# Kernel tuning notes

Hardware: AMD Instinct MI355X
Metric: run time of the kernel (lower is better)

The kernel has to match this reference:

```python
import jax, jax.numpy as jnp
import numpy as np

B = 131072      # number of graphs
P = 22          # num_players (pad/truncate target)
F = 14          # num_features
N = B * P       # total nodes
H1, H2 = 256, 128


def setup_inputs() -> dict:
    key = jax.random.key(0)
    ks = jax.random.split(key, 8)
    x = jax.random.normal(ks[0], (N, F), dtype=jnp.float32)
    batch = jnp.sort(jax.random.randint(ks[1], (N,), 0, B, dtype=jnp.int32))
    s1 = 1.0 / np.sqrt(P * F)
    s2 = 1.0 / np.sqrt(H1)
    s3 = 1.0 / np.sqrt(H2)
    W1 = jax.random.uniform(ks[2], (H1, P * F), jnp.float32, -s1, s1)
    b1 = jax.random.uniform(ks[3], (H1,), jnp.float32, -s1, s1)
    W2 = jax.random.uniform(ks[4], (H2, H1), jnp.float32, -s2, s2)
    b2 = jax.random.uniform(ks[5], (H2,), jnp.float32, -s2, s2)
    W3 = jax.random.uniform(ks[6], (P, H2), jnp.float32, -s3, s3)
    b3 = jax.random.uniform(ks[7], (P,), jnp.float32, -s3, s3)
    return {"x": x, "batch": batch, "W1": W1, "b1": b1, "W2": W2, "b2": b2, "W3": W3, "b3": b3}


def _flatten_batch(x, batch):
    # Vectorized equivalent of the per-graph mask/slice/pad loop.
    counts = jax.ops.segment_sum(jnp.ones((N,), jnp.int32), batch, num_segments=B)
    starts = jnp.concatenate([jnp.zeros((1,), jnp.int32), jnp.cumsum(counts)[:-1].astype(jnp.int32)])
    pos = jnp.arange(N, dtype=jnp.int32) - starts[batch]  # position within own graph
    # nodes beyond the first P per graph are truncated -> route to dump slot P
    slot = jnp.where(pos < P, pos, P)
    buf = jnp.zeros((B, P + 1, F), dtype=x.dtype)          # zero padding for short graphs
    buf = buf.at[batch, slot].set(x)
    return buf[:, :P, :].reshape(B, P * F)


def reference(x, batch, W1, b1, W2, b2, W3, b3):
    flat = _flatten_batch(x, batch)                        # [B, 308]
    h1 = jax.nn.relu(flat @ W1.T + b1)                     # dropout is eval-mode identity
    h2 = jax.nn.relu(h1 @ W2.T + b2)
    logits = h2 @ W3.T + b3                                # [B, 22]
    return logits
```

## Files before the change

kernel.cpp:

```cpp
#include <hip/hip_runtime.h>
#include <hip/hip_fp16.h>

typedef __attribute__((ext_vector_type(8))) _Float16 half8;
typedef __attribute__((ext_vector_type(4))) float f32x4;

namespace {
constexpr int B_G = 131072;
constexpr int P   = 22;
constexpr int F   = 14;
constexpr int NF  = 308;
constexpr long long N_NODES = (long long)B_G * P;

constexpr int G    = 48;
constexpr int NBLK = (B_G + G - 1) / G;

constexpr int KS1 = 10;
constexpr int KS2 = 8;
constexpr int KS3 = 4;
constexpr int JT1 = 16;
constexpr int JT2 = 8;
constexpr int JT3 = 2;

constexpr int W1F = 0;
constexpr int W2F = W1F + KS1 * JT1 * 1024;
constexpr int W3F = W2F + KS2 * JT2 * 1024;
constexpr int STARTS_OFF = W3F + KS3 * JT3 * 1024;
constexpr int CVT_DWORDS = (KS1*JT1 + KS2*JT2 + KS3*JT3) * 256;
constexpr int CVT_BLKS  = (CVT_DWORDS + 255) / 256;
constexpr int SCAN_BLKS = (int)((N_NODES + 255) / 256);

constexpr int A3O = 12288;
}

__device__ __forceinline__ unsigned short f2h(float v) {
    __half h = __float2half(v);
    return *reinterpret_cast<unsigned short*>(&h);
}

__global__ void aux_kernel(const float* __restrict__ W1,
                           const float* __restrict__ W2,
                           const float* __restrict__ W3,
                           const int* __restrict__ batch,
                           unsigned* __restrict__ ws,
                           int* __restrict__ starts)
{
    const int blk = blockIdx.x;
    const int t   = threadIdx.x;
    if (blk < CVT_BLKS) {
        int p = blk * 256 + t;
        if (p >= CVT_DWORDS) return;
        const int n1 = KS1 * JT1 * 256;
        const int n2 = KS2 * JT2 * 256;
        const float* W; int NK, NJ, stride, JT, oB, pl;
        if (p < n1)            { W = W1; NK = NF;  NJ = 256; stride = NF;  JT = JT1; oB = W1F/4; pl = p; }
        else if (p < n1 + n2)  { W = W2; NK = 256; NJ = 128; stride = 256; JT = JT2; oB = W2F/4; pl = p - n1; }
        else                   { W = W3; NK = 128; NJ = 22;  stride = 128; JT = JT3; oB = W3F/4; pl = p - n1 - n2; }

        const int e2   = pl & 3;
        const int lane = (pl >> 2) & 63;
        const int jt   = (pl >> 8) % JT;
        const int ks   = (pl >> 8) / JT;
        const int j    = jt * 16 + (lane & 15);
        const int kb   = ks * 32 + (lane >> 4) * 8 + e2 * 2;

        unsigned d = 0;
        #pragma unroll
        for (int q = 0; q < 2; ++q) {
            const int k = kb + q;
            const float v = (k < NK && j < NJ) ? W[j * stride + k] : 0.0f;
            d |= (unsigned)f2h(v) << (16 * q);
        }
        ws[oB + pl] = d;
    } else {
        const long long i = (long long)(blk - CVT_BLKS) * 256 + t;
        if (i >= N_NODES) return;
        const int b  = batch[i];
        const int bp = (i == 0) ? -1 : batch[i - 1];
        for (int g = bp + 1; g <= b; ++g) starts[g] = (int)i;
        if (i == N_NODES - 1)
            for (int g = b + 1; g <= B_G + G; ++g) starts[g] = (int)N_NODES;
    }
}

#define MFMA16(A_, B_, C_) __builtin_amdgcn_mfma_f32_16x16x32_f16(A_, B_, C_, 0, 0, 0)

#define LOADB1(H_, KS_) { \
    _Pragma("unroll") for (int n = 0; n < 4; ++n) \
        H_[n] = *reinterpret_cast<const half8*>(&B1[((((KS_) * JT1) + (wv * 4 + n)) * 64 + lane) * 8]); }

#define COMP1(H_, KS_) { \
    half8 a_[3]; \
    _Pragma("unroll") for (int m = 0; m < 3; ++m) \
        a_[m] = *reinterpret_cast<const half8*>(&s_scr[(((KS_) * 4 + kq) * G + (m * 16 + r16)) * 8]); \
    _Pragma("unroll") for (int n = 0; n < 4; ++n) \
        _Pragma("unroll") for (int m = 0; m < 3; ++m) \
            acc[m][n] = MFMA16(a_[m], H_[n], acc[m][n]); }

#define LOADB2(H_, KS_) { \
    _Pragma("unroll") for (int n = 0; n < 2; ++n) \
        H_[n] = *reinterpret_cast<const half8*>(&B2[((((KS_) * JT2) + (wv * 2 + n)) * 64 + lane) * 8]); }

#define COMP2(H_, KS_) { \
    half8 a_[3]; \
    _Pragma("unroll") for (int m = 0; m < 3; ++m) \
        a_[m] = *reinterpret_cast<const half8*>(&s_scr[(((KS_) * 4 + kq) * G + (m * 16 + r16)) * 8]); \
    _Pragma("unroll") for (int n = 0; n < 2; ++n) \
        _Pragma("unroll") for (int m = 0; m < 3; ++m) \
            acc2[m][n] = MFMA16(a_[m], H_[n], acc2[m][n]); }

#define GATHER_SLOT(ITEM_) { \
    const int it = (ITEM_); \
    const int g  = it / P; \
    const int p  = it - g * P; \
    const int s  = s_start[g]; \
    const int cnt = s_start[g + 1] - s; \
    const bool live = (p < cnt); \
    const float2* xr = reinterpret_cast<const float2*>(x + (size_t)(s + p) * F); \
    _Pragma("unroll") for (int q = 0; q < 7; ++q) { \
        float2 v = make_float2(0.f, 0.f); \
        if (live) v = xr[q]; \
        const int k = p * F + q * 2; \
        const unsigned d = (unsigned)f2h(v.x) | ((unsigned)f2h(v.y) << 16); \
        const int off = (((k >> 5) * 4 + ((k >> 3) & 3)) * G + g) * 8 + (k & 7); \
        *reinterpret_cast<unsigned*>(&s_scr[off]) = d; \
    } }

#define PIN8(V_) asm volatile("" :: "v"(V_))

__global__ __launch_bounds__(256, 4)
void mlp_mfma_kernel(const float* __restrict__ x,
                     const float* __restrict__ b1,
                     const float* __restrict__ b2,
                     const float* __restrict__ b3,
                     const unsigned short* __restrict__ ws,
                     const int* __restrict__ starts,
                     float* __restrict__ out)
{
    __shared__ __align__(16) unsigned short s_scr[18432];
    __shared__ float s_b1[256], s_b2[128], s_b3[32];
    __shared__ int s_start[G + 1];

    const int t    = threadIdx.x;
    const int g0   = blockIdx.x * G;
    const int lane = t & 63;
    const int wv   = t >> 6;
    const int r16  = lane & 15;
    const int kq   = lane >> 4;

    s_b1[t] = b1[t];
    if (t < 128) s_b2[t] = b2[t];
    if (t < 32)  s_b3[t] = (t < 22) ? b3[t] : 0.0f;

    if (t <= G) s_start[t] = starts[g0 + t];

    if (t < 192)
        reinterpret_cast<uint4*>(&s_scr[(9 * 4) * G * 8])[t] = make_uint4(0u, 0u, 0u, 0u);

    const unsigned short* B1 = ws + W1F / 2;
    const unsigned short* B2 = ws + W2F / 2;
    const unsigned short* B3 = ws + W3F / 2;

    half8 Ba[4], Bb[4], Bc[4];
    LOADB1(Ba, 0)
    LOADB1(Bb, 1)
    LOADB1(Bc, 2)
    __syncthreads();

    GATHER_SLOT(t)
    GATHER_SLOT(t + 256)
    GATHER_SLOT(t + 512)
    GATHER_SLOT(t + 768)
    if (t < 32) GATHER_SLOT(t + 1024)

    PIN8(Ba[0]); PIN8(Ba[1]); PIN8(Ba[2]); PIN8(Ba[3]);
    PIN8(Bb[0]); PIN8(Bb[1]); PIN8(Bb[2]); PIN8(Bb[3]);
    PIN8(Bc[0]); PIN8(Bc[1]); PIN8(Bc[2]); PIN8(Bc[3]);
    __syncthreads();

    f32x4 acc[3][4];
    #pragma unroll
    for (int m = 0; m < 3; ++m)
        #pragma unroll
        for (int n = 0; n < 4; ++n) acc[m][n] = (f32x4){0.f, 0.f, 0.f, 0.f};

    COMP1(Ba, 0)  LOADB1(Ba, 3)
    COMP1(Bb, 1)  LOADB1(Bb, 4)
    COMP1(Bc, 2)  LOADB1(Bc, 5)
    COMP1(Ba, 3)  LOADB1(Ba, 6)
    COMP1(Bb, 4)  LOADB1(Bb, 7)
    COMP1(Bc, 5)  LOADB1(Bc, 8)
    COMP1(Ba, 6)  LOADB1(Ba, 9)
    COMP1(Bb, 7)

    half8 Ca[2], Cb[2], Cc[2];
    LOADB2(Ca, 0)
    LOADB2(Cb, 1)
    LOADB2(Cc, 2)
    COMP1(Bc, 8)
    COMP1(Ba, 9)
    __syncthreads();

    #pragma unroll
    for (int n = 0; n < 4; ++n) {
        const int j = (wv * 4 + n) * 16 + r16;
        const float bb = s_b1[j];
        const int base = (((j >> 5) * 4 + ((j >> 3) & 3)) * G) * 8 + (j & 7);
        #pragma unroll
        for (int m = 0; m < 3; ++m)
            #pragma unroll
            for (int r = 0; r < 4; ++r) {
                const int g = m * 16 + kq * 4 + r;
                s_scr[base + g * 8] = f2h(fmaxf(acc[m][n][r] + bb, 0.0f));
            }
    }
    __syncthreads();

    f32x4 acc2[3][2];
    #pragma unroll
    for (int m = 0; m < 3; ++m)
        #pragma unroll
        for (int n = 0; n < 2; ++n) acc2[m][n] = (f32x4){0.f, 0.f, 0.f, 0.f};

    COMP2(Ca, 0)  LOADB2(Ca, 3)
    COMP2(Cb, 1)  LOADB2(Cb, 4)
    COMP2(Cc, 2)  LOADB2(Cc, 5)
    COMP2(Ca, 3)  LOADB2(Ca, 6)
    COMP2(Cb, 4)  LOADB2(Cb, 7)
    COMP2(Cc, 5)
    COMP2(Ca, 6)

    half8 D3[8];
    #pragma unroll
    for (int ks = 0; ks < KS3; ++ks)
        #pragma unroll
        for (int n = 0; n < 2; ++n)
            D3[ks * 2 + n] = *reinterpret_cast<const half8*>(&B3[((ks * JT3 + n) * 64 + lane) * 8]);
    COMP2(Cb, 7)

    #pragma unroll
    for (int n = 0; n < 2; ++n) {
        const int j = (wv * 2 + n) * 16 + r16;
        const float bb = s_b2[j];
        const int base = A3O + (((j >> 5) * 4 + ((j >> 3) & 3)) * G) * 8 + (j & 7);
        #pragma unroll
        for (int m = 0; m < 3; ++m)
            #pragma unroll
            for (int r = 0; r < 4; ++r) {
                const int g = m * 16 + kq * 4 + r;
                s_scr[base + g * 8] = f2h(fmaxf(acc2[m][n][r] + bb, 0.0f));
            }
    }
    __syncthreads();

    if (wv < 3) {
        f32x4 acc3[2];
        acc3[0] = (f32x4){0.f, 0.f, 0.f, 0.f};
        acc3[1] = (f32x4){0.f, 0.f, 0.f, 0.f};
        const int mg = wv * 16;
        #pragma unroll
        for (int ks = 0; ks < KS3; ++ks) {
            const half8 a = *reinterpret_cast<const half8*>(
                &s_scr[A3O + ((ks * 4 + kq) * G + (mg + r16)) * 8]);
            #pragma unroll
            for (int n = 0; n < 2; ++n)
                acc3[n] = MFMA16(a, D3[ks * 2 + n], acc3[n]);
        }
        #pragma unroll
        for (int n = 0; n < 2; ++n) {
            const int j = n * 16 + r16;
            if (j < P) {
                const float bb = s_b3[j];
                #pragma unroll
                for (int r = 0; r < 4; ++r) {
                    const int g = mg + kq * 4 + r;
                    if (g0 + g < B_G)
                        out[(size_t)(g0 + g) * P + j] = acc3[n][r] + bb;
                }
            }
        }
    }
}

extern "C" void kernel_launch(void* const* d_in, const int* in_sizes, int n_in,
                              void* d_out, int out_size, void* d_ws, size_t ws_size,
                              hipStream_t stream) {
    const float* x     = (const float*)d_in[0];
    const int*   batch = (const int*)  d_in[1];
    const float* W1    = (const float*)d_in[2];
    const float* b1    = (const float*)d_in[3];
    const float* W2    = (const float*)d_in[4];
    const float* b2    = (const float*)d_in[5];
    const float* W3    = (const float*)d_in[6];
    const float* b3    = (const float*)d_in[7];
    float* out = (float*)d_out;
    int* starts = (int*)((char*)d_ws + STARTS_OFF);

    aux_kernel<<<dim3(CVT_BLKS + SCAN_BLKS), dim3(256), 0, stream>>>(
        W1, W2, W3, batch, (unsigned*)d_ws, starts);
    mlp_mfma_kernel<<<dim3(NBLK), dim3(256), 0, stream>>>(
        x, b1, b2, b3, (const unsigned short*)d_ws, starts, out);
}
```

Before: 67.17 us.

## Make MLP kernel persistent with double-buffered prefetch of next tile's inputs

Changes the main kernel from one block per 48-graph tile to a persistent grid of 512 blocks that loop over tiles. The gather of the next tile's node features is issued into registers before the layer-1 MFMAs and written to a second LDS buffer afterwards, so global loads overlap compute. This doubles LDS use and lowers the occupancy target to 2 blocks per CU. Holding 56 floats per thread for the prefetch raises register pressure, and per-tile reloading of weights remains.

```diff
diff --git a/kernel.cpp b/kernel.cpp
--- a/kernel.cpp
+++ b/kernel.cpp
@@ -11,8 +11,9 @@
 constexpr int NF  = 308;
 constexpr long long N_NODES = (long long)B_G * P;
 
-constexpr int G    = 48;
-constexpr int NBLK = (B_G + G - 1) / G;
+constexpr int G     = 48;
+constexpr int TILES = (B_G + G - 1) / G;
+constexpr int NBLKP = 512;
 
 constexpr int KS1 = 10;
 constexpr int KS2 = 8;
@@ -29,7 +30,8 @@
 constexpr int CVT_BLKS  = (CVT_DWORDS + 255) / 256;
 constexpr int SCAN_BLKS = (int)((N_NODES + 255) / 256);
 
-constexpr int A3O = 12288;
+constexpr int A1SZ = 15360;
+constexpr int A3O  = 30720;
 }
 
 __device__ __forceinline__ unsigned short f2h(float v) {
@@ -91,7 +93,7 @@
 #define COMP1(H_, KS_) { \
     half8 a_[3]; \
     _Pragma("unroll") for (int m = 0; m < 3; ++m) \
-        a_[m] = *reinterpret_cast<const half8*>(&s_scr[(((KS_) * 4 + kq) * G + (m * 16 + r16)) * 8]); \
+        a_[m] = *reinterpret_cast<const half8*>(&s_scr[abase + (((KS_) * 4 + kq) * G + (m * 16 + r16)) * 8]); \
     _Pragma("unroll") for (int n = 0; n < 4; ++n) \
         _Pragma("unroll") for (int m = 0; m < 3; ++m) \
             acc[m][n] = MFMA16(a_[m], H_[n], acc[m][n]); }
@@ -103,31 +105,25 @@
 #define COMP2(H_, KS_) { \
     half8 a_[3]; \
     _Pragma("unroll") for (int m = 0; m < 3; ++m) \
-        a_[m] = *reinterpret_cast<const half8*>(&s_scr[(((KS_) * 4 + kq) * G + (m * 16 + r16)) * 8]); \
+        a_[m] = *reinterpret_cast<const half8*>(&s_scr[abase + (((KS_) * 4 + kq) * G + (m * 16 + r16)) * 8]); \
     _Pragma("unroll") for (int n = 0; n < 2; ++n) \
         _Pragma("unroll") for (int m = 0; m < 3; ++m) \
             acc2[m][n] = MFMA16(a_[m], H_[n], acc2[m][n]); }
 
-#define GATHER_SLOT(ITEM_) { \
-    const int it = (ITEM_); \
-    const int g  = it / P; \
-    const int p  = it - g * P; \
-    const int s  = s_start[g]; \
-    const int cnt = s_start[g + 1] - s; \
-    const bool live = (p < cnt); \
-    const float2* xr = reinterpret_cast<const float2*>(x + (size_t)(s + p) * F); \
+#define GSLOT_NOW(IT_, AB_, SBUF_) { \
+    const int g_ = (IT_) / P, p_ = (IT_) - g_ * P; \
+    const int s_ = SBUF_[g_], c_ = SBUF_[g_ + 1] - s_; \
+    const bool lv_ = (p_ < c_); \
+    const float2* xr_ = reinterpret_cast<const float2*>(x + (size_t)(s_ + p_) * F); \
     _Pragma("unroll") for (int q = 0; q < 7; ++q) { \
         float2 v = make_float2(0.f, 0.f); \
-        if (live) v = xr[q]; \
-        const int k = p * F + q * 2; \
+        if (lv_) v = xr_[q]; \
+        const int k = p_ * F + q * 2; \
         const unsigned d = (unsigned)f2h(v.x) | ((unsigned)f2h(v.y) << 16); \
-        const int off = (((k >> 5) * 4 + ((k >> 3) & 3)) * G + g) * 8 + (k & 7); \
-        *reinterpret_cast<unsigned*>(&s_scr[off]) = d; \
+        *reinterpret_cast<unsigned*>(&s_scr[(AB_) + (((k >> 5) * 4 + ((k >> 3) & 3)) * G + g_) * 8 + (k & 7)]) = d; \
     } }
 
-#define PIN8(V_) asm volatile("" :: "v"(V_))
-
-__global__ __launch_bounds__(256, 4)
+__global__ __launch_bounds__(256, 2)
 void mlp_mfma_kernel(const float* __restrict__ x,
                      const float* __restrict__ b1,
                      const float* __restrict__ b2,
@@ -136,12 +132,11 @@
                      const int* __restrict__ starts,
                      float* __restrict__ out)
 {
-    __shared__ __align__(16) unsigned short s_scr[18432];
+    __shared__ __align__(16) unsigned short s_scr[36864];
     __shared__ float s_b1[256], s_b2[128], s_b3[32];
-    __shared__ int s_start[G + 1];
+    __shared__ int s_st[2][G + 1];
 
     const int t    = threadIdx.x;
-    const int g0   = blockIdx.x * G;
     const int lane = t & 63;
     const int wv   = t >> 6;
     const int r16  = lane & 15;
@@ -151,133 +146,182 @@
     if (t < 128) s_b2[t] = b2[t];
     if (t < 32)  s_b3[t] = (t < 22) ? b3[t] : 0.0f;
 
-    if (t <= G) s_start[t] = starts[g0 + t];
-
-    if (t < 192)
-        reinterpret_cast<uint4*>(&s_scr[(9 * 4) * G * 8])[t] = make_uint4(0u, 0u, 0u, 0u);
-
     const unsigned short* B1 = ws + W1F / 2;
     const unsigned short* B2 = ws + W2F / 2;
     const unsigned short* B3 = ws + W3F / 2;
 
-    half8 Ba[4], Bb[4], Bc[4];
-    LOADB1(Ba, 0)
-    LOADB1(Bb, 1)
-    LOADB1(Bc, 2)
+    if (t < 96) {
+        const int c = t / 48, g = t % 48;
+        const int b38 = c * A1SZ + ((9 * 4 + 2) * G + g) * 8;
+        const int b39 = c * A1SZ + ((9 * 4 + 3) * G + g) * 8;
+        *reinterpret_cast<uint2*>(&s_scr[b38 + 4]) = make_uint2(0u, 0u);
+        *reinterpret_cast<uint2*>(&s_scr[b39])     = make_uint2(0u, 0u);
+        *reinterpret_cast<uint2*>(&s_scr[b39 + 4]) = make_uint2(0u, 0u);
+    }
+
+    int tile = blockIdx.x;
+    int cur  = 0;
+    if (t <= G) s_st[0][t] = starts[tile * G + t];
     __syncthreads();
 
-    GATHER_SLOT(t)
-    GATHER_SLOT(t + 256)
-    GATHER_SLOT(t + 512)
-    GATHER_SLOT(t + 768)
-    if (t < 32) GATHER_SLOT(t + 1024)
-
-    PIN8(Ba[0]); PIN8(Ba[1]); PIN8(Ba[2]); PIN8(Ba[3]);
-    PIN8(Bb[0]); PIN8(Bb[1]); PIN8(Bb[2]); PIN8(Bb[3]);
-    PIN8(Bc[0]); PIN8(Bc[1]); PIN8(Bc[2]); PIN8(Bc[3]);
-    __syncthreads();
-
-    f32x4 acc[3][4];
-    #pragma unroll
-    for (int m = 0; m < 3; ++m)
-        #pragma unroll
-        for (int n = 0; n < 4; ++n) acc[m][n] = (f32x4){0.f, 0.f, 0.f, 0.f};
-
-    COMP1(Ba, 0)  LOADB1(Ba, 3)
-    COMP1(Bb, 1)  LOADB1(Bb, 4)
-    COMP1(Bc, 2)  LOADB1(Bc, 5)
-    COMP1(Ba, 3)  LOADB1(Ba, 6)
-    COMP1(Bb, 4)  LOADB1(Bb, 7)
-    COMP1(Bc, 5)  LOADB1(Bc, 8)
-    COMP1(Ba, 6)  LOADB1(Ba, 9)
-    COMP1(Bb, 7)
-
-    half8 Ca[2], Cb[2], Cc[2];
-    LOADB2(Ca, 0)
-    LOADB2(Cb, 1)
-    LOADB2(Cc, 2)
-    COMP1(Bc, 8)
-    COMP1(Ba, 9)
-    __syncthreads();
-
-    #pragma unroll
-    for (int n = 0; n < 4; ++n) {
-        const int j = (wv * 4 + n) * 16 + r16;
-        const float bb = s_b1[j];
-        const int base = (((j >> 5) * 4 + ((j >> 3) & 3)) * G) * 8 + (j & 7);
+    GSLOT_NOW(t,       0, s_st[0])
+    GSLOT_NOW(t + 256, 0, s_st[0])
+    GSLOT_NOW(t + 512, 0, s_st[0])
+    GSLOT_NOW(t + 768, 0, s_st[0])
+    if (t < 32) GSLOT_NOW(t + 1024, 0, s_st[0])
+
+    for (; tile < TILES; tile += NBLKP) {
+        const int  g0    = tile * G;
+        const int  tileN = tile + NBLKP;
+        const bool hasN  = (tileN < TILES);
+        const int  nxt   = cur ^ 1;
+        const int  abase = cur * A1SZ;
+        const int  nbase = nxt * A1SZ;
+
+        half8 Ba[4], Bb[4], Bc[4];
+        LOADB1(Ba, 0)
+        LOADB1(Bb, 1)
+        LOADB1(Bc, 2)
+        if (hasN && t <= G) s_st[nxt][t] = starts[tileN * G + t];
+        __syncthreads();
+
+        float2 xv[4][7];
+        int gu[4], pu[4];
+        if (hasN) {
+            const int* sn = s_st[nxt];
+            #pragma unroll
+            for (int u = 0; u < 4; ++u) {
+                const int it = t + u * 256;
+                const int g_ = it / P, p_ = it - g_ * P;
+                gu[u] = g_; pu[u] = p_;
+                const int s_ = sn[g_], c_ = sn[g_ + 1] - s_;
+                const bool lv = (p_ < c_);
+                const float2* xr = reinterpret_cast<const float2*>(x + (size_t)(s_ + p_) * F);
+                #pragma unroll
+                for (int q = 0; q < 7; ++q) {
+                    xv[u][q] = make_float2(0.f, 0.f);
+                    if (lv) xv[u][q] = xr[q];
+                }
+            }
+        }
+
+        f32x4 acc[3][4];
         #pragma unroll
         for (int m = 0; m < 3; ++m)
             #pragma unroll
-            for (int r = 0; r < 4; ++r) {
-                const int g = m * 16 + kq * 4 + r;
-                s_scr[base + g * 8] = f2h(fmaxf(acc[m][n][r] + bb, 0.0f));
+            for (int n = 0; n < 4; ++n) acc[m][n] = (f32x4){0.f, 0.f, 0.f, 0.f};
+
+        COMP1(Ba, 0)  LOADB1(Ba, 3)
+        COMP1(Bb, 1)  LOADB1(Bb, 4)
+        COMP1(Bc, 2)  LOADB1(Bc, 5)
+        COMP1(Ba, 3)  LOADB1(Ba, 6)
+        COMP1(Bb, 4)  LOADB1(Bb, 7)
+        COMP1(Bc, 5)  LOADB1(Bc, 8)
+        COMP1(Ba, 6)  LOADB1(Ba, 9)
+        COMP1(Bb, 7)
+
+        half8 Ca[2], Cb[2], Cc[2];
+        LOADB2(Ca, 0)
+        LOADB2(Cb, 1)
+        LOADB2(Cc, 2)
+        COMP1(Bc, 8)
+        COMP1(Ba, 9)
+        __syncthreads();
+
+        #pragma unroll
+        for (int n = 0; n < 4; ++n) {
+            const int j = (wv * 4 + n) * 16 + r16;
+            const float bb = s_b1[j];
+            const int base = abase + (((j >> 5) * 4 + ((j >> 3) & 3)) * G) * 8 + (j & 7);
+            #pragma unroll
+            for (int m = 0; m < 3; ++m)
+                #pragma unroll
+                for (int r = 0; r < 4; ++r) {
+                    const int g = m * 16 + kq * 4 + r;
+                    s_scr[base + g * 8] = f2h(fmaxf(acc[m][n][r] + bb, 0.0f));
+                }
+        }
+        __syncthreads();
+
+        if (hasN) {
+            #pragma unroll
+            for (int u = 0; u < 4; ++u) {
+                #pragma unroll
+                for (int q = 0; q < 7; ++q) {
+                    const int k = pu[u] * F + q * 2;
+                    const unsigned d = (unsigned)f2h(xv[u][q].x) | ((unsigned)f2h(xv[u][q].y) << 16);
+                    *reinterpret_cast<unsigned*>(
+                        &s_scr[nbase + (((k >> 5) * 4 + ((k >> 3) & 3)) * G + gu[u]) * 8 + (k & 7)]) = d;
+                }
             }
-    }
-    __syncthreads();
-
-    f32x4 acc2[3][2];
-    #pragma unroll
-    for (int m = 0; m < 3; ++m)
-        #pragma unroll
-        for (int n = 0; n < 2; ++n) acc2[m][n] = (f32x4){0.f, 0.f, 0.f, 0.f};
-
-    COMP2(Ca, 0)  LOADB2(Ca, 3)
-    COMP2(Cb, 1)  LOADB2(Cb, 4)
-    COMP2(Cc, 2)  LOADB2(Cc, 5)
-    COMP2(Ca, 3)  LOADB2(Ca, 6)
-    COMP2(Cb, 4)  LOADB2(Cb, 7)
-    COMP2(Cc, 5)
-    COMP2(Ca, 6)
-
-    half8 D3[8];
-    #pragma unroll
-    for (int ks = 0; ks < KS3; ++ks)
-        #pragma unroll
-        for (int n = 0; n < 2; ++n)
-            D3[ks * 2 + n] = *reinterpret_cast<const half8*>(&B3[((ks * JT3 + n) * 64 + lane) * 8]);
-    COMP2(Cb, 7)
-
-    #pragma unroll
-    for (int n = 0; n < 2; ++n) {
-        const int j = (wv * 2 + n) * 16 + r16;
-        const float bb = s_b2[j];
-        const int base = A3O + (((j >> 5) * 4 + ((j >> 3) & 3)) * G) * 8 + (j & 7);
+            if (t < 32) GSLOT_NOW(t + 1024, nbase, s_st[nxt])
+        }
+
+        f32x4 acc2[3][2];
         #pragma unroll
         for (int m = 0; m < 3; ++m)
             #pragma unroll
-            for (int r = 0; r < 4; ++r) {
-                const int g = m * 16 + kq * 4 + r;
-                s_scr[base + g * 8] = f2h(fmaxf(acc2[m][n][r] + bb, 0.0f));
+            for (int n = 0; n < 2; ++n) acc2[m][n] = (f32x4){0.f, 0.f, 0.f, 0.f};
+
+        COMP2(Ca, 0)  LOADB2(Ca, 3)
+        COMP2(Cb, 1)  LOADB2(Cb, 4)
+        COMP2(Cc, 2)  LOADB2(Cc, 5)
+        COMP2(Ca, 3)  LOADB2(Ca, 6)
+        COMP2(Cb, 4)  LOADB2(Cb, 7)
+        COMP2(Cc, 5)
+        COMP2(Ca, 6)
+
+        half8 D3[8];
+        #pragma unroll
+        for (int ks = 0; ks < KS3; ++ks)
+            #pragma unroll
+            for (int n = 0; n < 2; ++n)
+                D3[ks * 2 + n] = *reinterpret_cast<const half8*>(&B3[((ks * JT3 + n) * 64 + lane) * 8]);
+        COMP2(Cb, 7)
+
+        #pragma unroll
+        for (int n = 0; n < 2; ++n) {
+            const int j = (wv * 2 + n) * 16 + r16;
+            const float bb = s_b2[j];
+            const int base = A3O + (((j >> 5) * 4 + ((j >> 3) & 3)) * G) * 8 + (j & 7);
+            #pragma unroll
+            for (int m = 0; m < 3; ++m)
+                #pragma unroll
+                for (int r = 0; r < 4; ++r) {
+                    const int g = m * 16 + kq * 4 + r;
+                    s_scr[base + g * 8] = f2h(fmaxf(acc2[m][n][r] + bb, 0.0f));
+                }
+        }
+        __syncthreads();
+
+        if (wv < 3) {
+            f32x4 acc3[2];
+            acc3[0] = (f32x4){0.f, 0.f, 0.f, 0.f};
+            acc3[1] = (f32x4){0.f, 0.f, 0.f, 0.f};
+            const int mg = wv * 16;
+            #pragma unroll
+            for (int ks = 0; ks < KS3; ++ks) {
+                const half8 a = *reinterpret_cast<const half8*>(
+                    &s_scr[A3O + ((ks * 4 + kq) * G + (mg + r16)) * 8]);
+                #pragma unroll
+                for (int n = 0; n < 2; ++n)
+                    acc3[n] = MFMA16(a, D3[ks * 2 + n], acc3[n]);
             }
-    }
-    __syncthreads();
-
-    if (wv < 3) {
-        f32x4 acc3[2];
-        acc3[0] = (f32x4){0.f, 0.f, 0.f, 0.f};
-        acc3[1] = (f32x4){0.f, 0.f, 0.f, 0.f};
-        const int mg = wv * 16;
-        #pragma unroll
-        for (int ks = 0; ks < KS3; ++ks) {
-            const half8 a = *reinterpret_cast<const half8*>(
-                &s_scr[A3O + ((ks * 4 + kq) * G + (mg + r16)) * 8]);
-            #pragma unroll
-            for (int n = 0; n < 2; ++n)
-                acc3[n] = MFMA16(a, D3[ks * 2 + n], acc3[n]);
-        }
-        #pragma unroll
-        for (int n = 0; n < 2; ++n) {
-            const int j = n * 16 + r16;
-            if (j < P) {
-                const float bb = s_b3[j];
-                #pragma unroll
-                for (int r = 0; r < 4; ++r) {
-                    const int g = mg + kq * 4 + r;
-                    if (g0 + g < B_G)
-                        out[(size_t)(g0 + g) * P + j] = acc3[n][r] + bb;
+            #pragma unroll
+            for (int n = 0; n < 2; ++n) {
+                const int j = n * 16 + r16;
+                if (j < P) {
+                    const float bb = s_b3[j];
+                    #pragma unroll
+                    for (int r = 0; r < 4; ++r) {
+                        const int g = mg + kq * 4 + r;
+                        if (g0 + g < B_G)
+                            out[(size_t)(g0 + g) * P + j] = acc3[n][r] + bb;
+                    }
                 }
             }
         }
+        cur = nxt;
     }
 }
 
@@ -297,6 +341,6 @@
 
     aux_kernel<<<dim3(CVT_BLKS + SCAN_BLKS), dim3(256), 0, stream>>>(
         W1, W2, W3, batch, (unsigned*)d_ws, starts);
-    mlp_mfma_kernel<<<dim3(NBLK), dim3(256), 0, stream>>>(
+    mlp_mfma_kernel<<<dim3(NBLKP), dim3(256), 0, stream>>>(
         x, b1, b2, b3, (const unsigned short*)d_ws, starts, out);
 }
```

After: 209.7 us. +212.3%, slower.
